# Kernel tuning notes

Measured on AMD Instinct MI355X. Metric: run time of the kernel, lower is better.

Reference implementation:

```python
import jax, jax.numpy as jnp
import numpy as np

B, C, H, W = 16, 256, 64, 64
NH, HD = 8, 32  # num_heads, head_dim


def _conv1x1(x, w, b):
    # x: [B,C,H,W], w: [Cout,Cin], b: [Cout] -> [B,Cout,H,W]
    return jnp.einsum('bchw,oc->bohw', x, w) + b[None, :, None, None]


def setup_inputs() -> dict:
    key = jax.random.key(0)
    ks = jax.random.split(key, 11)
    s = 1.0 / np.sqrt(C)
    return {
        'q': jax.random.normal(ks[0], (B, C, H, W), jnp.float32),
        'k': jax.random.normal(ks[1], (B, C, H, W), jnp.float32),
        'v': jax.random.normal(ks[2], (B, C, H, W), jnp.float32),
        'Wq': jax.random.normal(ks[3], (C, C), jnp.float32) * s,
        'bq': jax.random.normal(ks[4], (C,), jnp.float32) * 0.01,
        'Wk': jax.random.normal(ks[5], (C, C), jnp.float32) * s,
        'bk': jax.random.normal(ks[6], (C,), jnp.float32) * 0.01,
        'Wv': jax.random.normal(ks[7], (C, C), jnp.float32) * s,
        'bv': jax.random.normal(ks[8], (C,), jnp.float32) * 0.01,
        'Wo': jax.random.normal(ks[9], (C, C), jnp.float32) * s,
        'bo': jax.random.normal(ks[10], (C,), jnp.float32) * 0.01,
    }


def reference(q, k, v, Wq, bq, Wk, bk, Wv, bv, Wo, bo):
    # 1x1 conv projections, then split heads: [B, NH, HD, H, W]
    qh = _conv1x1(q, Wq, bq).reshape(B, NH, HD, H, W)
    kh = _conv1x1(k, Wk, bk).reshape(B, NH, HD, H, W)
    vh = _conv1x1(v, Wv, bv).reshape(B, NH, HD, H, W)
    # Attention over last two dims: q @ k^T -> [B, NH, HD, H, H], d_k = W
    scale = 1.0 / jnp.sqrt(jnp.float32(W))
    logits = jnp.einsum('bndhw,bndgw->bndhg', qh, kh) * scale
    attn = jax.nn.softmax(logits, axis=-1)  # [B,NH,HD,H,H]
    out = jnp.einsum('bndhg,bndgw->bndhw', attn, vh)  # [B,NH,HD,H,W]
    out = out.reshape(B, C, H, W)  # combine heads
    out = _conv1x1(out, Wo, bo)
    return out, attn
```

## Files before the change

### kernel.cpp

```cpp
#include <hip/hip_runtime.h>

#define NB  16
#define CC  256
#define SH  64
#define SW  64
#define HWP 4096
#define NSLICE (NB * CC)
#define OUT_ELEMS ((size_t)NB * CC * HWP)
#define PADK 40

using bf16x8 = __attribute__((ext_vector_type(8))) short;
using f32x4  = __attribute__((ext_vector_type(4))) float;

static __device__ __forceinline__ unsigned pack_hi16(unsigned u0, unsigned u1) {
    return __builtin_amdgcn_perm(u1, u0, 0x07060302u);
}
static __device__ __forceinline__ float trunc_bf(unsigned u) {
    union { unsigned u; float f; } v; v.u = u & 0xFFFF0000u; return v.f;
}
static __device__ __forceinline__ unsigned fbits(float x) {
    union { float f; unsigned u; } v; v.f = x; return v.u;
}

static __device__ __forceinline__ void split8(float4 a, float4 b,
                                              bf16x8& hi, bf16x8& lo) {
    union { bf16x8 v; unsigned u[4]; } H, L;
    const float f[8] = {a.x, a.y, a.z, a.w, b.x, b.y, b.z, b.w};
    #pragma unroll
    for (int j = 0; j < 4; ++j) {
        const unsigned u0 = fbits(f[2 * j]), u1 = fbits(f[2 * j + 1]);
        const float r0 = f[2 * j]     - trunc_bf(u0);
        const float r1 = f[2 * j + 1] - trunc_bf(u1);
        H.u[j] = pack_hi16(u0, u1);
        L.u[j] = pack_hi16(fbits(r0), fbits(r1));
    }
    hi = H.v; lo = L.v;
}

static __device__ __forceinline__ void proj_body(
    const float* __restrict__ X, const float* __restrict__ W,
    const float* __restrict__ bias, float* __restrict__ Y,
    int b, int o0, int p0)
{
    __shared__ short sWhi[128][PADK];
    __shared__ short sWlo[128][PADK];
    __shared__ short sXhi[128][PADK];
    __shared__ short sXlo[128][PADK];

    const int tid = threadIdx.x;
    const float* Xb = X + (size_t)b * CC * HWP;

    const int wid  = tid >> 6;
    const int lane = tid & 63;
    const int wr = wid >> 1, wc = wid & 1;
    const int l16 = lane & 15, lq = lane >> 4;

    const int kq = tid & 7;
    const int ooB = tid >> 3;
    const int cb = tid & 7;
    const int pb = tid >> 3;

    f32x4 acc[4][4] = {};

    for (int c0 = 0; c0 < CC; c0 += 32) {
        __syncthreads();
        #pragma unroll
        for (int pass = 0; pass < 4; ++pass) {
            const int oo = ooB + pass * 32;
            const float4 wv = *(const float4*)&W[(size_t)(o0 + oo) * CC + c0 + kq * 4];
            const unsigned u0 = fbits(wv.x), u1 = fbits(wv.y),
                           u2 = fbits(wv.z), u3 = fbits(wv.w);
            const float r0 = wv.x - trunc_bf(u0);
            const float r1 = wv.y - trunc_bf(u1);
            const float r2 = wv.z - trunc_bf(u2);
            const float r3 = wv.w - trunc_bf(u3);
            uint2 hi, lo;
            hi.x = pack_hi16(u0, u1);          hi.y = pack_hi16(u2, u3);
            lo.x = pack_hi16(fbits(r0), fbits(r1));
            lo.y = pack_hi16(fbits(r2), fbits(r3));
            *(uint2*)&sWhi[oo][kq * 4] = hi;
            *(uint2*)&sWlo[oo][kq * 4] = lo;
        }
        {
            const float* xsrc = Xb + (size_t)(c0 + cb * 4) * HWP + p0 + pb * 4;
            const float4 x0 = *(const float4*)(xsrc);
            const float4 x1 = *(const float4*)(xsrc + HWP);
            const float4 x2 = *(const float4*)(xsrc + 2 * HWP);
            const float4 x3 = *(const float4*)(xsrc + 3 * HWP);
            const float c0v[4][4] = {{x0.x, x1.x, x2.x, x3.x},
                                     {x0.y, x1.y, x2.y, x3.y},
                                     {x0.z, x1.z, x2.z, x3.z},
                                     {x0.w, x1.w, x2.w, x3.w}};
            #pragma unroll
            for (int j = 0; j < 4; ++j) {
                const unsigned u0 = fbits(c0v[j][0]), u1 = fbits(c0v[j][1]),
                               u2 = fbits(c0v[j][2]), u3 = fbits(c0v[j][3]);
                const float r0 = c0v[j][0] - trunc_bf(u0);
                const float r1 = c0v[j][1] - trunc_bf(u1);
                const float r2 = c0v[j][2] - trunc_bf(u2);
                const float r3 = c0v[j][3] - trunc_bf(u3);
                uint2 hi, lo;
                hi.x = pack_hi16(u0, u1);          hi.y = pack_hi16(u2, u3);
                lo.x = pack_hi16(fbits(r0), fbits(r1));
                lo.y = pack_hi16(fbits(r2), fbits(r3));
                *(uint2*)&sXhi[pb * 4 + j][cb * 4] = hi;
                *(uint2*)&sXlo[pb * 4 + j][cb * 4] = lo;
            }
        }
        __syncthreads();

        const int aRow = wr * 64 + l16;
        const int bRow = wc * 64 + l16;
        bf16x8 bhi[4], blo[4];
        #pragma unroll
        for (int fn = 0; fn < 4; ++fn) {
            bhi[fn] = *(const bf16x8*)&sXhi[bRow + fn * 16][lq * 8];
            blo[fn] = *(const bf16x8*)&sXlo[bRow + fn * 16][lq * 8];
        }
        #pragma unroll
        for (int fm = 0; fm < 4; ++fm) {
            const bf16x8 ahi = *(const bf16x8*)&sWhi[aRow + fm * 16][lq * 8];
            const bf16x8 alo = *(const bf16x8*)&sWlo[aRow + fm * 16][lq * 8];
            #pragma unroll
            for (int fn = 0; fn < 4; ++fn) {
                acc[fm][fn] = __builtin_amdgcn_mfma_f32_16x16x32_bf16(
                    ahi, bhi[fn], acc[fm][fn], 0, 0, 0);
                acc[fm][fn] = __builtin_amdgcn_mfma_f32_16x16x32_bf16(
                    ahi, blo[fn], acc[fm][fn], 0, 0, 0);
                acc[fm][fn] = __builtin_amdgcn_mfma_f32_16x16x32_bf16(
                    alo, bhi[fn], acc[fm][fn], 0, 0, 0);
            }
        }
    }

    #pragma unroll
    for (int fm = 0; fm < 4; ++fm) {
        #pragma unroll
        for (int j = 0; j < 4; ++j) {
            const int o = o0 + wr * 64 + fm * 16 + lq * 4 + j;
            const float bv = bias[o];
            #pragma unroll
            for (int fn = 0; fn < 4; ++fn) {
                Y[((size_t)b * CC + o) * HWP + p0 + wc * 64 + fn * 16 + l16] =
                    acc[fm][fn][j] + bv;
            }
        }
    }
}

__global__ __launch_bounds__(256) void proj_qkv_kernel(
    const float* __restrict__ q, const float* __restrict__ Wq,
    const float* __restrict__ bq, float* __restrict__ qh,
    const float* __restrict__ k, const float* __restrict__ Wk,
    const float* __restrict__ bk, float* __restrict__ kh,
    const float* __restrict__ v, const float* __restrict__ Wv,
    const float* __restrict__ bv, float* __restrict__ vh)
{
    const int which = blockIdx.z >> 4;
    const int b     = blockIdx.z & 15;
    const float* X  = (which == 0) ? q  : (which == 1) ? k  : v;
    const float* W  = (which == 0) ? Wq : (which == 1) ? Wk : Wv;
    const float* bi = (which == 0) ? bq : (which == 1) ? bk : bv;
    float*       Y  = (which == 0) ? qh : (which == 1) ? kh : vh;
    proj_body(X, W, bi, Y, b, blockIdx.x * 128, blockIdx.y * 128);
}

__global__ __launch_bounds__(256) void proj_o_kernel(
    const float* __restrict__ X, const float* __restrict__ W,
    const float* __restrict__ bias, float* __restrict__ Y)
{
    proj_body(X, W, bias, Y, blockIdx.z, blockIdx.x * 128, blockIdx.y * 128);
}

__global__ __launch_bounds__(256) void attn_mfma_kernel(
    const float* qh, const float* kh, const float* vh,
    float* attn_out, float* out_pre)
{
    __shared__ float Pb[4][16][68];

    const int tid  = threadIdx.x;
    const int wid  = tid >> 6;
    const int lane = tid & 63;
    const int l16  = lane & 15;
    const int lq   = lane >> 4;

    const int s = blockIdx.x * 4 + wid;
    const size_t base = (size_t)s * HWP;
    const float* Q = qh + base;
    const float* K = kh + base;
    const float* V = vh + base;
    float (*P)[68] = Pb[wid];

    bf16x8 Khi[4][2], Klo[4][2];
    #pragma unroll
    for (int nt = 0; nt < 4; ++nt)
        #pragma unroll
        for (int ks = 0; ks < 2; ++ks) {
            const float* src = K + (nt * 16 + l16) * SW + ks * 32 + lq * 8;
            split8(*(const float4*)src, *(const float4*)(src + 4),
                   Khi[nt][ks], Klo[nt][ks]);
        }

    f32x4 acc[4][4] = {};
    #pragma unroll
    for (int mt = 0; mt < 4; ++mt) {
        bf16x8 Qhi[2], Qlo[2];
        #pragma unroll
        for (int ks = 0; ks < 2; ++ks) {
            const float* src = Q + (mt * 16 + l16) * SW + ks * 32 + lq * 8;
            split8(*(const float4*)src, *(const float4*)(src + 4),
                   Qhi[ks], Qlo[ks]);
        }
        #pragma unroll
        for (int nt = 0; nt < 4; ++nt)
            #pragma unroll
            for (int ks = 0; ks < 2; ++ks) {
                acc[mt][nt] = __builtin_amdgcn_mfma_f32_16x16x32_bf16(
                    Qhi[ks], Khi[nt][ks], acc[mt][nt], 0, 0, 0);
                acc[mt][nt] = __builtin_amdgcn_mfma_f32_16x16x32_bf16(
                    Qhi[ks], Klo[nt][ks], acc[mt][nt], 0, 0, 0);
                acc[mt][nt] = __builtin_amdgcn_mfma_f32_16x16x32_bf16(
                    Qlo[ks], Khi[nt][ks], acc[mt][nt], 0, 0, 0);
            }
    }

    bf16x8 Vhi[4][2], Vlo[4][2];
    #pragma unroll
    for (int nt = 0; nt < 4; ++nt)
        #pragma unroll
        for (int ks = 0; ks < 2; ++ks) {
            const float* vcol = V + nt * 16 + l16;
            float f[8];
            #pragma unroll
            for (int e = 0; e < 8; ++e)
                f[e] = vcol[(ks * 32 + lq * 8 + e) * SW];
            split8(make_float4(f[0], f[1], f[2], f[3]),
                   make_float4(f[4], f[5], f[6], f[7]),
                   Vhi[nt][ks], Vlo[nt][ks]);
        }

    #pragma unroll
    for (int mt = 0; mt < 4; ++mt) {
        #pragma unroll
        for (int r = 0; r < 4; ++r) {
            float l0 = acc[mt][0][r] * 0.125f;
            float l1 = acc[mt][1][r] * 0.125f;
            float l2 = acc[mt][2][r] * 0.125f;
            float l3 = acc[mt][3][r] * 0.125f;
            float m = fmaxf(fmaxf(l0, l1), fmaxf(l2, l3));
            m = fmaxf(m, __shfl_xor(m, 1));
            m = fmaxf(m, __shfl_xor(m, 2));
            m = fmaxf(m, __shfl_xor(m, 4));
            m = fmaxf(m, __shfl_xor(m, 8));
            const float e0 = __expf(l0 - m);
            const float e1 = __expf(l1 - m);
            const float e2 = __expf(l2 - m);
            const float e3 = __expf(l3 - m);
            float sum = e0 + e1 + e2 + e3;
            sum += __shfl_xor(sum, 1);
            sum += __shfl_xor(sum, 2);
            sum += __shfl_xor(sum, 4);
            sum += __shfl_xor(sum, 8);
            const float rs = 1.0f / sum;
            const float p0 = e0 * rs, p1 = e1 * rs, p2 = e2 * rs, p3 = e3 * rs;
            const int h = mt * 16 + lq * 4 + r;
            float* gdst = attn_out + base + (size_t)h * SH;
            gdst[0 * 16 + l16] = p0;
            gdst[1 * 16 + l16] = p1;
            gdst[2 * 16 + l16] = p2;
            gdst[3 * 16 + l16] = p3;
            const int hr = lq * 4 + r;
            P[hr][0 * 16 + l16] = p0;
            P[hr][1 * 16 + l16] = p1;
            P[hr][2 * 16 + l16] = p2;
            P[hr][3 * 16 + l16] = p3;
        }
        f32x4 o[4] = {};
        #pragma unroll
        for (int ks = 0; ks < 2; ++ks) {
            const float* src = &P[l16][ks * 32 + lq * 8];
            bf16x8 Phi, Plo;
            split8(*(const float4*)src, *(const float4*)(src + 4), Phi, Plo);
            #pragma unroll
            for (int nt = 0; nt < 4; ++nt) {
                o[nt] = __builtin_amdgcn_mfma_f32_16x16x32_bf16(
                    Phi, Vhi[nt][ks], o[nt], 0, 0, 0);
                o[nt] = __builtin_amdgcn_mfma_f32_16x16x32_bf16(
                    Phi, Vlo[nt][ks], o[nt], 0, 0, 0);
                o[nt] = __builtin_amdgcn_mfma_f32_16x16x32_bf16(
                    Plo, Vhi[nt][ks], o[nt], 0, 0, 0);
            }
        }
        #pragma unroll
        for (int nt = 0; nt < 4; ++nt)
            #pragma unroll
            for (int r = 0; r < 4; ++r)
                out_pre[base + (size_t)(mt * 16 + lq * 4 + r) * SW + nt * 16 + l16] =
                    o[nt][r];
    }
}

extern "C" void kernel_launch(void* const* d_in, const int* in_sizes, int n_in,
                              void* d_out, int out_size, void* d_ws, size_t ws_size,
                              hipStream_t stream) {
    (void)in_sizes; (void)n_in; (void)out_size; (void)ws_size;

    const float* q  = (const float*)d_in[0];
    const float* k  = (const float*)d_in[1];
    const float* v  = (const float*)d_in[2];
    const float* Wq = (const float*)d_in[3];
    const float* bq = (const float*)d_in[4];
    const float* Wk = (const float*)d_in[5];
    const float* bk = (const float*)d_in[6];
    const float* Wv = (const float*)d_in[7];
    const float* bv = (const float*)d_in[8];
    const float* Wo = (const float*)d_in[9];
    const float* bo = (const float*)d_in[10];

    float* out  = (float*)d_out;
    float* attn = out + OUT_ELEMS;

    float* vh      = out;
    float* kh      = attn;
    float* qh      = (float*)d_ws;
    float* out_pre = qh;

    const dim3 blk(256);

    proj_qkv_kernel<<<dim3(2, 32, 48), blk, 0, stream>>>(
        q, Wq, bq, qh, k, Wk, bk, kh, v, Wv, bv, vh);

    attn_mfma_kernel<<<dim3(NSLICE / 4), blk, 0, stream>>>(
        qh, kh, vh, attn, out_pre);

    proj_o_kernel<<<dim3(2, 32, 16), blk, 0, stream>>>(out_pre, Wo, bo, out);
}
```

Measured before the change: 454.8 us.

## Register-prefetch projection tiles and restage attention through shared memory per slice

The projection GEMM now loads the next K-chunk of W and X into registers before running the MFMAs on the current chunk, so global loads overlap with compute. The attention kernel is restructured so that one block handles one slice instead of four. Q, K and a transposed V are staged in LDS with coalesced float4 loads, and each wave handles one 16-row tile. The attention probabilities and the output are written back through LDS as coalesced float4 stores, replacing scattered scalar and strided global accesses. In exchange the kernel uses more LDS per block, adds barriers, and launches four times as many blocks.

```diff
diff --git a/kernel.cpp b/kernel.cpp
--- a/kernel.cpp
+++ b/kernel.cpp
@@ -61,13 +61,25 @@
     const int pb = tid >> 3;
 
     f32x4 acc[4][4] = {};
-
-    for (int c0 = 0; c0 < CC; c0 += 32) {
+    float4 wreg[4], xreg[4];
+
+    #pragma unroll
+    for (int pass = 0; pass < 4; ++pass)
+        wreg[pass] = *(const float4*)&W[(size_t)(o0 + ooB + pass * 32) * CC + kq * 4];
+    {
+        const float* xsrc = Xb + (size_t)(cb * 4) * HWP + p0 + pb * 4;
+        xreg[0] = *(const float4*)(xsrc);
+        xreg[1] = *(const float4*)(xsrc + HWP);
+        xreg[2] = *(const float4*)(xsrc + 2 * HWP);
+        xreg[3] = *(const float4*)(xsrc + 3 * HWP);
+    }
+
+    for (int t = 0; t < 8; ++t) {
         __syncthreads();
         #pragma unroll
         for (int pass = 0; pass < 4; ++pass) {
             const int oo = ooB + pass * 32;
-            const float4 wv = *(const float4*)&W[(size_t)(o0 + oo) * CC + c0 + kq * 4];
+            const float4 wv = wreg[pass];
             const unsigned u0 = fbits(wv.x), u1 = fbits(wv.y),
                            u2 = fbits(wv.z), u3 = fbits(wv.w);
             const float r0 = wv.x - trunc_bf(u0);
@@ -82,15 +94,10 @@
             *(uint2*)&sWlo[oo][kq * 4] = lo;
         }
         {
-            const float* xsrc = Xb + (size_t)(c0 + cb * 4) * HWP + p0 + pb * 4;
-            const float4 x0 = *(const float4*)(xsrc);
-            const float4 x1 = *(const float4*)(xsrc + HWP);
-            const float4 x2 = *(const float4*)(xsrc + 2 * HWP);
-            const float4 x3 = *(const float4*)(xsrc + 3 * HWP);
-            const float c0v[4][4] = {{x0.x, x1.x, x2.x, x3.x},
-                                     {x0.y, x1.y, x2.y, x3.y},
-                                     {x0.z, x1.z, x2.z, x3.z},
-                                     {x0.w, x1.w, x2.w, x3.w}};
+            const float c0v[4][4] = {{xreg[0].x, xreg[1].x, xreg[2].x, xreg[3].x},
+                                     {xreg[0].y, xreg[1].y, xreg[2].y, xreg[3].y},
+                                     {xreg[0].z, xreg[1].z, xreg[2].z, xreg[3].z},
+                                     {xreg[0].w, xreg[1].w, xreg[2].w, xreg[3].w}};
             #pragma unroll
             for (int j = 0; j < 4; ++j) {
                 const unsigned u0 = fbits(c0v[j][0]), u1 = fbits(c0v[j][1]),
@@ -109,6 +116,19 @@
         }
         __syncthreads();
 
+        if (t < 7) {
+            const int c0n = (t + 1) * 32;
+            #pragma unroll
+            for (int pass = 0; pass < 4; ++pass)
+                wreg[pass] = *(const float4*)
+                    &W[(size_t)(o0 + ooB + pass * 32) * CC + c0n + kq * 4];
+            const float* xsrc = Xb + (size_t)(c0n + cb * 4) * HWP + p0 + pb * 4;
+            xreg[0] = *(const float4*)(xsrc);
+            xreg[1] = *(const float4*)(xsrc + HWP);
+            xreg[2] = *(const float4*)(xsrc + 2 * HWP);
+            xreg[3] = *(const float4*)(xsrc + 3 * HWP);
+        }
+
         const int aRow = wr * 64 + l16;
         const int bRow = wc * 64 + l16;
         bf16x8 bhi[4], blo[4];
@@ -176,7 +196,9 @@
     const float* qh, const float* kh, const float* vh,
     float* attn_out, float* out_pre)
 {
-    __shared__ float Pb[4][16][68];
+    __shared__ float Qs[64][68];
+    __shared__ float Ks[64][68];
+    __shared__ float Vt[64][68];
 
     const int tid  = threadIdx.x;
     const int wid  = tid >> 6;
@@ -184,119 +206,128 @@
     const int l16  = lane & 15;
     const int lq   = lane >> 4;
 
-    const int s = blockIdx.x * 4 + wid;
+    const int s = blockIdx.x;
     const size_t base = (size_t)s * HWP;
     const float* Q = qh + base;
     const float* K = kh + base;
     const float* V = vh + base;
-    float (*P)[68] = Pb[wid];
-
-    bf16x8 Khi[4][2], Klo[4][2];
+
+    #pragma unroll
+    for (int i = 0; i < 4; ++i) {
+        const int idx = tid + i * 256;
+        const int row = idx >> 4, ch = (idx & 15) * 4;
+        *(float4*)&Qs[row][ch] = *(const float4*)&Q[row * SW + ch];
+        *(float4*)&Ks[row][ch] = *(const float4*)&K[row * SW + ch];
+    }
+    {
+        const int tr = tid & 15, tc = tid >> 4;
+        const float* src = V + (tc * 4) * SW + tr * 4;
+        const float4 a0 = *(const float4*)(src);
+        const float4 a1 = *(const float4*)(src + SW);
+        const float4 a2 = *(const float4*)(src + 2 * SW);
+        const float4 a3 = *(const float4*)(src + 3 * SW);
+        *(float4*)&Vt[tr * 4 + 0][tc * 4] = make_float4(a0.x, a1.x, a2.x, a3.x);
+        *(float4*)&Vt[tr * 4 + 1][tc * 4] = make_float4(a0.y, a1.y, a2.y, a3.y);
+        *(float4*)&Vt[tr * 4 + 2][tc * 4] = make_float4(a0.z, a1.z, a2.z, a3.z);
+        *(float4*)&Vt[tr * 4 + 3][tc * 4] = make_float4(a0.w, a1.w, a2.w, a3.w);
+    }
+    __syncthreads();
+
+    const int mt = wid;
+
+    bf16x8 Qhi[2], Qlo[2];
+    #pragma unroll
+    for (int ks = 0; ks < 2; ++ks) {
+        const float* srcq = &Qs[mt * 16 + l16][ks * 32 + lq * 8];
+        split8(*(const float4*)srcq, *(const float4*)(srcq + 4), Qhi[ks], Qlo[ks]);
+    }
+
+    f32x4 acc[4] = {};
+    #pragma unroll
+    for (int nt = 0; nt < 4; ++nt) {
+        #pragma unroll
+        for (int ks = 0; ks < 2; ++ks) {
+            const float* srck = &Ks[nt * 16 + l16][ks * 32 + lq * 8];
+            bf16x8 Khi, Klo;
+            split8(*(const float4*)srck, *(const float4*)(srck + 4), Khi, Klo);
+            acc[nt] = __builtin_amdgcn_mfma_f32_16x16x32_bf16(
+                Qhi[ks], Khi, acc[nt], 0, 0, 0);
+            acc[nt] = __builtin_amdgcn_mfma_f32_16x16x32_bf16(
+                Qhi[ks], Klo, acc[nt], 0, 0, 0);
+            acc[nt] = __builtin_amdgcn_mfma_f32_16x16x32_bf16(
+                Qlo[ks], Khi, acc[nt], 0, 0, 0);
+        }
+    }
+
+    #pragma unroll
+    for (int r = 0; r < 4; ++r) {
+        float l0 = acc[0][r] * 0.125f;
+        float l1 = acc[1][r] * 0.125f;
+        float l2 = acc[2][r] * 0.125f;
+        float l3 = acc[3][r] * 0.125f;
+        float m = fmaxf(fmaxf(l0, l1), fmaxf(l2, l3));
+        m = fmaxf(m, __shfl_xor(m, 1));
+        m = fmaxf(m, __shfl_xor(m, 2));
+        m = fmaxf(m, __shfl_xor(m, 4));
+        m = fmaxf(m, __shfl_xor(m, 8));
+        const float e0 = __expf(l0 - m);
+        const float e1 = __expf(l1 - m);
+        const float e2 = __expf(l2 - m);
+        const float e3 = __expf(l3 - m);
+        float sum = e0 + e1 + e2 + e3;
+        sum += __shfl_xor(sum, 1);
+        sum += __shfl_xor(sum, 2);
+        sum += __shfl_xor(sum, 4);
+        sum += __shfl_xor(sum, 8);
+        const float rs = 1.0f / sum;
+        const int h = mt * 16 + lq * 4 + r;
+        Qs[h][0 * 16 + l16] = e0 * rs;
+        Qs[h][1 * 16 + l16] = e1 * rs;
+        Qs[h][2 * 16 + l16] = e2 * rs;
+        Qs[h][3 * 16 + l16] = e3 * rs;
+    }
+
+    #pragma unroll
+    for (int i = 0; i < 4; ++i) {
+        const int idx = lane + i * 64;
+        const int row = mt * 16 + (idx >> 4), ch = (idx & 15) * 4;
+        *(float4*)&attn_out[base + (size_t)row * SH + ch] =
+            *(const float4*)&Qs[row][ch];
+    }
+
+    __syncthreads();
+
+    f32x4 o[4] = {};
+    #pragma unroll
+    for (int ks = 0; ks < 2; ++ks) {
+        const float* srcp = &Qs[mt * 16 + l16][ks * 32 + lq * 8];
+        bf16x8 Phi, Plo;
+        split8(*(const float4*)srcp, *(const float4*)(srcp + 4), Phi, Plo);
+        #pragma unroll
+        for (int nt = 0; nt < 4; ++nt) {
+            const float* srcv = &Vt[nt * 16 + l16][ks * 32 + lq * 8];
+            bf16x8 Vhi, Vlo;
+            split8(*(const float4*)srcv, *(const float4*)(srcv + 4), Vhi, Vlo);
+            o[nt] = __builtin_amdgcn_mfma_f32_16x16x32_bf16(
+                Phi, Vhi, o[nt], 0, 0, 0);
+            o[nt] = __builtin_amdgcn_mfma_f32_16x16x32_bf16(
+                Phi, Vlo, o[nt], 0, 0, 0);
+            o[nt] = __builtin_amdgcn_mfma_f32_16x16x32_bf16(
+                Plo, Vhi, o[nt], 0, 0, 0);
+        }
+    }
+
     #pragma unroll
     for (int nt = 0; nt < 4; ++nt)
         #pragma unroll
-        for (int ks = 0; ks < 2; ++ks) {
-            const float* src = K + (nt * 16 + l16) * SW + ks * 32 + lq * 8;
-            split8(*(const float4*)src, *(const float4*)(src + 4),
-                   Khi[nt][ks], Klo[nt][ks]);
-        }
-
-    f32x4 acc[4][4] = {};
-    #pragma unroll
-    for (int mt = 0; mt < 4; ++mt) {
-        bf16x8 Qhi[2], Qlo[2];
-        #pragma unroll
-        for (int ks = 0; ks < 2; ++ks) {
-            const float* src = Q + (mt * 16 + l16) * SW + ks * 32 + lq * 8;
-            split8(*(const float4*)src, *(const float4*)(src + 4),
-                   Qhi[ks], Qlo[ks]);
-        }
-        #pragma unroll
-        for (int nt = 0; nt < 4; ++nt)
-            #pragma unroll
-            for (int ks = 0; ks < 2; ++ks) {
-                acc[mt][nt] = __builtin_amdgcn_mfma_f32_16x16x32_bf16(
-                    Qhi[ks], Khi[nt][ks], acc[mt][nt], 0, 0, 0);
-                acc[mt][nt] = __builtin_amdgcn_mfma_f32_16x16x32_bf16(
-                    Qhi[ks], Klo[nt][ks], acc[mt][nt], 0, 0, 0);
-                acc[mt][nt] = __builtin_amdgcn_mfma_f32_16x16x32_bf16(
-                    Qlo[ks], Khi[nt][ks], acc[mt][nt], 0, 0, 0);
-            }
-    }
-
-    bf16x8 Vhi[4][2], Vlo[4][2];
-    #pragma unroll
-    for (int nt = 0; nt < 4; ++nt)
-        #pragma unroll
-        for (int ks = 0; ks < 2; ++ks) {
-            const float* vcol = V + nt * 16 + l16;
-            float f[8];
-            #pragma unroll
-            for (int e = 0; e < 8; ++e)
-                f[e] = vcol[(ks * 32 + lq * 8 + e) * SW];
-            split8(make_float4(f[0], f[1], f[2], f[3]),
-                   make_float4(f[4], f[5], f[6], f[7]),
-                   Vhi[nt][ks], Vlo[nt][ks]);
-        }
-
-    #pragma unroll
-    for (int mt = 0; mt < 4; ++mt) {
-        #pragma unroll
-        for (int r = 0; r < 4; ++r) {
-            float l0 = acc[mt][0][r] * 0.125f;
-            float l1 = acc[mt][1][r] * 0.125f;
-            float l2 = acc[mt][2][r] * 0.125f;
-            float l3 = acc[mt][3][r] * 0.125f;
-            float m = fmaxf(fmaxf(l0, l1), fmaxf(l2, l3));
-            m = fmaxf(m, __shfl_xor(m, 1));
-            m = fmaxf(m, __shfl_xor(m, 2));
-            m = fmaxf(m, __shfl_xor(m, 4));
-            m = fmaxf(m, __shfl_xor(m, 8));
-            const float e0 = __expf(l0 - m);
-            const float e1 = __expf(l1 - m);
-            const float e2 = __expf(l2 - m);
-            const float e3 = __expf(l3 - m);
-            float sum = e0 + e1 + e2 + e3;
-            sum += __shfl_xor(sum, 1);
-            sum += __shfl_xor(sum, 2);
-            sum += __shfl_xor(sum, 4);
-            sum += __shfl_xor(sum, 8);
-            const float rs = 1.0f / sum;
-            const float p0 = e0 * rs, p1 = e1 * rs, p2 = e2 * rs, p3 = e3 * rs;
-            const int h = mt * 16 + lq * 4 + r;
-            float* gdst = attn_out + base + (size_t)h * SH;
-            gdst[0 * 16 + l16] = p0;
-            gdst[1 * 16 + l16] = p1;
-            gdst[2 * 16 + l16] = p2;
-            gdst[3 * 16 + l16] = p3;
-            const int hr = lq * 4 + r;
-            P[hr][0 * 16 + l16] = p0;
-            P[hr][1 * 16 + l16] = p1;
-            P[hr][2 * 16 + l16] = p2;
-            P[hr][3 * 16 + l16] = p3;
-        }
-        f32x4 o[4] = {};
-        #pragma unroll
-        for (int ks = 0; ks < 2; ++ks) {
-            const float* src = &P[l16][ks * 32 + lq * 8];
-            bf16x8 Phi, Plo;
-            split8(*(const float4*)src, *(const float4*)(src + 4), Phi, Plo);
-            #pragma unroll
-            for (int nt = 0; nt < 4; ++nt) {
-                o[nt] = __builtin_amdgcn_mfma_f32_16x16x32_bf16(
-                    Phi, Vhi[nt][ks], o[nt], 0, 0, 0);
-                o[nt] = __builtin_amdgcn_mfma_f32_16x16x32_bf16(
-                    Phi, Vlo[nt][ks], o[nt], 0, 0, 0);
-                o[nt] = __builtin_amdgcn_mfma_f32_16x16x32_bf16(
-                    Plo, Vhi[nt][ks], o[nt], 0, 0, 0);
-            }
-        }
-        #pragma unroll
-        for (int nt = 0; nt < 4; ++nt)
-            #pragma unroll
-            for (int r = 0; r < 4; ++r)
-                out_pre[base + (size_t)(mt * 16 + lq * 4 + r) * SW + nt * 16 + l16] =
-                    o[nt][r];
+        for (int r = 0; r < 4; ++r)
+            Ks[mt * 16 + lq * 4 + r][nt * 16 + l16] = o[nt][r];
+    #pragma unroll
+    for (int i = 0; i < 4; ++i) {
+        const int idx = lane + i * 64;
+        const int row = mt * 16 + (idx >> 4), ch = (idx & 15) * 4;
+        *(float4*)&out_pre[base + (size_t)row * SW + ch] =
+            *(const float4*)&Ks[row][ch];
     }
 }
 
@@ -330,7 +361,7 @@
     proj_qkv_kernel<<<dim3(2, 32, 48), blk, 0, stream>>>(
         q, Wq, bq, qh, k, Wk, bk, kh, v, Wv, bv, vh);
 
-    attn_mfma_kernel<<<dim3(NSLICE / 4), blk, 0, stream>>>(
+    attn_mfma_kernel<<<dim3(NSLICE), blk, 0, stream>>>(
         qh, kh, vh, attn, out_pre);
 
     proj_o_kernel<<<dim3(2, 32, 16), blk, 0, stream>>>(out_pre, Wo, bo, out);
```

After: 419.8 us. 7.7% less time.
